# Performance work log

Hardware: AMD Instinct MI355X
Metric: run time of the kernel (lower is better)

## Reference

```python
import jax, jax.numpy as jnp
import numpy as np

N_NODES = 100000
N_EDGES = 800000
IN_DIM = 128
HID = 128
N_CLASSES = 4


def setup_inputs() -> dict:
    key = jax.random.key(0)
    ks = jax.random.split(key, 8)
    x = jax.random.normal(ks[0], (N_NODES, IN_DIM), dtype=jnp.float32)
    edge_index = jax.random.randint(ks[1], (2, N_EDGES), 0, N_NODES, dtype=jnp.int32)
    s0 = 1.0 / np.sqrt(IN_DIM)
    s1 = 1.0 / np.sqrt(HID)
    W0 = jax.random.uniform(ks[2], (HID, IN_DIM), minval=-s0, maxval=s0, dtype=jnp.float32)
    b0 = jax.random.uniform(ks[3], (HID,), minval=-s0, maxval=s0, dtype=jnp.float32)
    W1 = jax.random.uniform(ks[4], (HID, HID), minval=-s1, maxval=s1, dtype=jnp.float32)
    b1 = jax.random.uniform(ks[5], (HID,), minval=-s1, maxval=s1, dtype=jnp.float32)
    Wc = jax.random.uniform(ks[6], (N_CLASSES, HID), minval=-s1, maxval=s1, dtype=jnp.float32)
    bc = jax.random.uniform(ks[7], (N_CLASSES,), minval=-s1, maxval=s1, dtype=jnp.float32)
    return {"x": x, "edge_index": edge_index, "W0": W0, "b0": b0,
            "W1": W1, "b1": b1, "Wc": Wc, "bc": bc}


def reference(x, edge_index, W0, b0, W1, b1, Wc, bc):
    row, col = edge_index[0], edge_index[1]
    n = x.shape[0]
    # layer 0: Linear + ReLU (dropout is identity in eval)
    h = jax.nn.relu(x @ W0.T + b0)                                  # [N, HID]
    # scatter-add neighbor aggregation with degree normalization
    agg = jax.ops.segment_sum(h[col], row, num_segments=n)          # [N, HID]
    deg = jax.ops.segment_sum(jnp.ones_like(row, dtype=h.dtype), row, num_segments=n)
    agg = agg / jnp.clip(deg, 1.0)[:, None]
    h = h + agg                                                     # residual add
    # final conv + ReLU + classifier
    h = jax.nn.relu(h @ W1.T + b1)
    logits = h @ Wc.T + bc                                          # [N, N_CLASSES]
    return logits
```

## Files before the change

kernel.cpp:

```cpp
#include <hip/hip_runtime.h>

#define IN_DIM 128
#define HID    128
#define NCLS   4

typedef __attribute__((ext_vector_type(8))) short bf16x8;
typedef __attribute__((ext_vector_type(4))) float f32x4;

__device__ inline ushort f2bf(float x) {
    uint u = __builtin_bit_cast(uint, x);
    u += 0x7FFFu + ((u >> 16) & 1u);
    return (ushort)(u >> 16);
}
__device__ inline float bf2f(ushort h) {
    uint u = ((uint)h) << 16;
    return __builtin_bit_cast(float, u);
}

__device__ inline void gload_lds16(const void* g, void* l) {
    __builtin_amdgcn_global_load_lds((const __attribute__((address_space(1))) void*)g,
                                     (__attribute__((address_space(3))) void*)l, 16, 0, 0);
}

__global__ __launch_bounds__(256) void cast_w(const float* __restrict__ W0,
                                              const float* __restrict__ W1,
                                              ushort* __restrict__ w0h, ushort* __restrict__ w0l,
                                              ushort* __restrict__ w1h, ushort* __restrict__ w1l)
{
    int i = blockIdx.x * 256 + threadIdx.x;
    float v = (i < 16384) ? W0[i] : W1[i - 16384];
    ushort h = f2bf(v);
    ushort l = f2bf(v - bf2f(h));
    if (i < 16384) { w0h[i] = h; w0l[i] = l; }
    else           { w1h[i - 16384] = h; w1l[i - 16384] = l; }
}


__device__ __forceinline__ void lin0_body(const float* __restrict__ X,
                                          const ushort* __restrict__ Whi,
                                          const ushort* __restrict__ Wlo,
                                          const float* __restrict__ Bv,
                                          ushort* __restrict__ Hhi,
                                          ushort* __restrict__ Hlo,
                                          int M, int bm, char* lds)
{
    const int tid = threadIdx.x;

    {
        const int row  = tid >> 2;
        const int seg  = tid & 3;
        const int grow = min(bm + row, M - 1);
        const float4* src = (const float4*)((const char*)X + (size_t)grow * 512 + seg * 128);
        float4 v[8];
        #pragma unroll
        for (int j = 0; j < 8; ++j) v[j] = src[j];

        #pragma unroll
        for (int j = 0; j < 4; ++j) {
            uint hw[4], lw[4];
            #pragma unroll
            for (int q = 0; q < 2; ++q) {
                const float4 f = v[j * 2 + q];
                ushort h0 = f2bf(f.x), h1 = f2bf(f.y), h2 = f2bf(f.z), h3 = f2bf(f.w);
                ushort l0 = f2bf(f.x - bf2f(h0)), l1 = f2bf(f.y - bf2f(h1));
                ushort l2 = f2bf(f.z - bf2f(h2)), l3 = f2bf(f.w - bf2f(h3));
                hw[q * 2]     = (uint)h0 | ((uint)h1 << 16);
                hw[q * 2 + 1] = (uint)h2 | ((uint)h3 << 16);
                lw[q * 2]     = (uint)l0 | ((uint)l1 << 16);
                lw[q * 2 + 1] = (uint)l2 | ((uint)l3 << 16);
            }
            int unit = (seg * 4 + j) ^ (row & 7);
            int off  = row * 256 + unit * 16;
            *(uint4*)(lds + off)         = make_uint4(hw[0], hw[1], hw[2], hw[3]);
            *(uint4*)(lds + 16384 + off) = make_uint4(lw[0], lw[1], lw[2], lw[3]);
        }
    }
    __syncthreads();

    const int wid = tid >> 6, lane = tid & 63;
    const int wr = wid >> 1, wc = wid & 1;
    const int colbase = wc * 64;
    const int lr = lane & 15, lk = lane >> 4;

    f32x4 acc[4][2];
    #pragma unroll
    for (int nt = 0; nt < 4; ++nt)
        #pragma unroll
        for (int rt = 0; rt < 2; ++rt) acc[nt][rt] = (f32x4){0.f, 0.f, 0.f, 0.f};

    #pragma unroll
    for (int kt = 0; kt < 4; ++kt) {
        const int ko = kt * 32 + lk * 8;
        bf16x8 xh[2], xl[2];
        #pragma unroll
        for (int rt = 0; rt < 2; ++rt) {
            int lrow = wr * 32 + rt * 16 + lr;
            int unit = (kt * 4 + lk) ^ (lrow & 7);
            int off  = lrow * 256 + unit * 16;
            xh[rt] = *(const bf16x8*)(lds + off);
            xl[rt] = *(const bf16x8*)(lds + 16384 + off);
        }
        #pragma unroll
        for (int nt = 0; nt < 4; ++nt) {
            size_t bo = (size_t)(colbase + nt * 16 + lr) * 128 + ko;
            bf16x8 wh = *(const bf16x8*)(Whi + bo);
            bf16x8 wl = *(const bf16x8*)(Wlo + bo);
            #pragma unroll
            for (int rt = 0; rt < 2; ++rt) {
                acc[nt][rt] = __builtin_amdgcn_mfma_f32_16x16x32_bf16(wh, xh[rt], acc[nt][rt], 0, 0, 0);
                acc[nt][rt] = __builtin_amdgcn_mfma_f32_16x16x32_bf16(wh, xl[rt], acc[nt][rt], 0, 0, 0);
                acc[nt][rt] = __builtin_amdgcn_mfma_f32_16x16x32_bf16(wl, xh[rt], acc[nt][rt], 0, 0, 0);
            }
        }
    }

    #pragma unroll
    for (int nt = 0; nt < 4; ++nt) {
        const int col0 = colbase + nt * 16 + lk * 4;
        const float4 bv4 = *(const float4*)(Bv + col0);
        const float bvv[4] = {bv4.x, bv4.y, bv4.z, bv4.w};
        #pragma unroll
        for (int rt = 0; rt < 2; ++rt) {
            int row = bm + wr * 32 + rt * 16 + lr;
            float o0 = fmaxf(acc[nt][rt][0] + bvv[0], 0.f);
            float o1 = fmaxf(acc[nt][rt][1] + bvv[1], 0.f);
            float o2 = fmaxf(acc[nt][rt][2] + bvv[2], 0.f);
            float o3 = fmaxf(acc[nt][rt][3] + bvv[3], 0.f);
            ushort4 h4, l4;
            h4.x = f2bf(o0); l4.x = f2bf(o0 - bf2f(h4.x));
            h4.y = f2bf(o1); l4.y = f2bf(o1 - bf2f(h4.y));
            h4.z = f2bf(o2); l4.z = f2bf(o2 - bf2f(h4.z));
            h4.w = f2bf(o3); l4.w = f2bf(o3 - bf2f(h4.w));
            size_t oo = (size_t)row * 128 + col0;
            *(ushort4*)(Hhi + oo) = h4;
            *(ushort4*)(Hlo + oo) = l4;
        }
    }
}

__global__ __launch_bounds__(256) void k_lin0_count(const float* __restrict__ X,
                                                    const ushort* __restrict__ Whi,
                                                    const ushort* __restrict__ Wlo,
                                                    const float* __restrict__ Bv,
                                                    ushort* __restrict__ Hhi,
                                                    ushort* __restrict__ Hlo, int M,
                                                    int nLin0,
                                                    const int* __restrict__ rows,
                                                    int* __restrict__ deg, int E)
{
    __shared__ uint4 lds4[2048];
    if ((int)blockIdx.x < nLin0) {
        lin0_body(X, Whi, Wlo, Bv, Hhi, Hlo, M, blockIdx.x * 64, (char*)lds4);
    } else {
        int e = (blockIdx.x - nLin0) * 256 + threadIdx.x;
        if (e < E) atomicAdd(&deg[rows[e]], 1);
    }
}

__global__ __launch_bounds__(256) void k_lin0_fill(const float* __restrict__ X,
                                                   const ushort* __restrict__ Whi,
                                                   const ushort* __restrict__ Wlo,
                                                   const float* __restrict__ Bv,
                                                   ushort* __restrict__ Hhi,
                                                   ushort* __restrict__ Hlo, int M,
                                                   int nLin0, int baseLin0,
                                                   const int* __restrict__ rows,
                                                   const int* __restrict__ cols,
                                                   int* __restrict__ pos,
                                                   int* __restrict__ col_sorted, int E)
{
    __shared__ uint4 lds4[2048];
    if ((int)blockIdx.x < nLin0) {
        lin0_body(X, Whi, Wlo, Bv, Hhi, Hlo, M, (baseLin0 + blockIdx.x) * 64, (char*)lds4);
    } else {
        int e = (blockIdx.x - nLin0) * 256 + threadIdx.x;
        if (e < E) {
            int p = atomicAdd(&pos[rows[e]], 1);
            __builtin_nontemporal_store(cols[e], &col_sorted[p]);
        }
    }
}

__global__ __launch_bounds__(256) void gnn_lin1_mfma(const ushort* __restrict__ Ahi,
                                                     const ushort* __restrict__ Alo,
                                                     const ushort* __restrict__ Whi,
                                                     const ushort* __restrict__ Wlo,
                                                     const float* __restrict__ Bv,
                                                     const float* __restrict__ Wc,
                                                     const float* __restrict__ bc,
                                                     float* __restrict__ Out, int M)
{
    __shared__ uint4 lds4[2048];
    __shared__ float red[2][64][4];
    char* lds = (char*)lds4;

    const int tid = threadIdx.x;
    const int wid = tid >> 6, lane = tid & 63;
    const int bm  = blockIdx.x * 64;

    #pragma unroll
    for (int i = 0; i < 8; ++i) {
        int o = wid * 8192 + i * 1024 + lane * 16;
        const ushort* plane = (o < 16384) ? Ahi : Alo;
        int po   = o & 16383;
        int row  = po >> 8;
        int unit = (po >> 4) & 15;
        const char* src = (const char*)plane + (size_t)(bm + row) * 256
                        + ((unit ^ (row & 7)) << 4);
        gload_lds16(src, lds + wid * 8192 + i * 1024);
    }
    __syncthreads();

    const int wr = wid >> 1, wc = wid & 1;
    const int colbase = wc * 64;
    const int lr = lane & 15, lk = lane >> 4;

    f32x4 acc[4][2];
    #pragma unroll
    for (int nt = 0; nt < 4; ++nt)
        #pragma unroll
        for (int rt = 0; rt < 2; ++rt) acc[nt][rt] = (f32x4){0.f, 0.f, 0.f, 0.f};

    #pragma unroll
    for (int kt = 0; kt < 4; ++kt) {
        const int ko = kt * 32 + lk * 8;
        bf16x8 xh[2], xl[2];
        #pragma unroll
        for (int rt = 0; rt < 2; ++rt) {
            int lrow = wr * 32 + rt * 16 + lr;
            int unit = (kt * 4 + lk) ^ (lrow & 7);
            int off  = lrow * 256 + unit * 16;
            xh[rt] = *(const bf16x8*)(lds + off);
            xl[rt] = *(const bf16x8*)(lds + 16384 + off);
        }
        #pragma unroll
        for (int nt = 0; nt < 4; ++nt) {
            size_t bo = (size_t)(colbase + nt * 16 + lr) * 128 + ko;
            bf16x8 wh = *(const bf16x8*)(Whi + bo);
            bf16x8 wl = *(const bf16x8*)(Wlo + bo);
            #pragma unroll
            for (int rt = 0; rt < 2; ++rt) {
                acc[nt][rt] = __builtin_amdgcn_mfma_f32_16x16x32_bf16(wh, xh[rt], acc[nt][rt], 0, 0, 0);
                acc[nt][rt] = __builtin_amdgcn_mfma_f32_16x16x32_bf16(wh, xl[rt], acc[nt][rt], 0, 0, 0);
                acc[nt][rt] = __builtin_amdgcn_mfma_f32_16x16x32_bf16(wl, xh[rt], acc[nt][rt], 0, 0, 0);
            }
        }
    }

    float p[2][4] = {{0.f, 0.f, 0.f, 0.f}, {0.f, 0.f, 0.f, 0.f}};
    #pragma unroll
    for (int nt = 0; nt < 4; ++nt) {
        const int col0 = colbase + nt * 16 + lk * 4;
        const float4 bv4 = *(const float4*)(Bv + col0);
        const float bvv[4] = {bv4.x, bv4.y, bv4.z, bv4.w};
        float4 wcr[4];
        #pragma unroll
        for (int c = 0; c < 4; ++c) wcr[c] = *(const float4*)(Wc + c * HID + col0);
        #pragma unroll
        for (int rt = 0; rt < 2; ++rt) {
            float h2v[4];
            #pragma unroll
            for (int r = 0; r < 4; ++r) h2v[r] = fmaxf(acc[nt][rt][r] + bvv[r], 0.f);
            #pragma unroll
            for (int c = 0; c < 4; ++c) {
                const float* w = (const float*)&wcr[c];
                p[rt][c] = fmaf(h2v[0], w[0], p[rt][c]);
                p[rt][c] = fmaf(h2v[1], w[1], p[rt][c]);
                p[rt][c] = fmaf(h2v[2], w[2], p[rt][c]);
                p[rt][c] = fmaf(h2v[3], w[3], p[rt][c]);
            }
        }
    }
    #pragma unroll
    for (int offs = 16; offs < 64; offs <<= 1)
        #pragma unroll
        for (int rt = 0; rt < 2; ++rt)
            #pragma unroll
            for (int c = 0; c < 4; ++c)
                p[rt][c] += __shfl_xor(p[rt][c], offs);

    if (lk == 0) {
        #pragma unroll
        for (int rt = 0; rt < 2; ++rt) {
            f32x4 v = {p[rt][0], p[rt][1], p[rt][2], p[rt][3]};
            *(f32x4*)&red[wc][wr * 32 + rt * 16 + lr][0] = v;
        }
    }
    __syncthreads();

    const int row_local = tid >> 2, cls = tid & 3;
    int row = blockIdx.x * 64 + row_local;
    if (row < M) {
        float s = bc[cls] + red[0][row_local][cls] + red[1][row_local][cls];
        Out[(size_t)row * 4 + cls] = s;
    }
}

__global__ __launch_bounds__(256) void scan_blocks(const int* __restrict__ deg,
                                                   int* __restrict__ off,
                                                   int* __restrict__ bsum, int M)
{
    __shared__ int sh[256];
    int i = blockIdx.x * 256 + threadIdx.x;
    int v = (i < M) ? deg[i] : 0;
    sh[threadIdx.x] = v;
    __syncthreads();
    #pragma unroll
    for (int d = 1; d < 256; d <<= 1) {
        int t = (threadIdx.x >= d) ? sh[threadIdx.x - d] : 0;
        __syncthreads();
        sh[threadIdx.x] += t;
        __syncthreads();
    }
    if (i < M) off[i] = sh[threadIdx.x] - v;
    if (threadIdx.x == 255) bsum[blockIdx.x] = sh[255];
}

__global__ __launch_bounds__(512) void scan_bsum(int* __restrict__ bsum, int NB)
{
    __shared__ int sh[512];
    int v = (threadIdx.x < NB) ? bsum[threadIdx.x] : 0;
    sh[threadIdx.x] = v;
    __syncthreads();
    #pragma unroll
    for (int d = 1; d < 512; d <<= 1) {
        int t = (threadIdx.x >= d) ? sh[threadIdx.x - d] : 0;
        __syncthreads();
        sh[threadIdx.x] += t;
        __syncthreads();
    }
    if (threadIdx.x < NB) bsum[threadIdx.x] = sh[threadIdx.x] - v;
}

__global__ __launch_bounds__(256) void add_off(int* __restrict__ off,
                                               const int* __restrict__ bsum,
                                               int* __restrict__ pos, int M)
{
    int i = blockIdx.x * 256 + threadIdx.x;
    if (i < M) {
        int o = off[i] + bsum[i >> 8];
        off[i] = o;
        pos[i] = o;
    }
}

__global__ __launch_bounds__(256) void gnn_aggregate(const ushort* __restrict__ Hhi,
                                                     const ushort* __restrict__ Hlo,
                                                     const int* __restrict__ off,
                                                     const int* __restrict__ deg,
                                                     const int* __restrict__ col_sorted,
                                                     ushort* __restrict__ InHi,
                                                     ushort* __restrict__ InLo,
                                                     int M, int Mpad)
{
    int gid  = blockIdx.x * 8 + (threadIdx.x >> 5);
    int lane = threadIdx.x & 31;
    if (gid >= Mpad) return;
    size_t oidx = (size_t)gid * 32 + lane;
    if (gid >= M) {
        ((ushort4*)InHi)[oidx] = make_ushort4(0, 0, 0, 0);
        ((ushort4*)InLo)[oidx] = make_ushort4(0, 0, 0, 0);
        return;
    }

    const ushort4* G = (const ushort4*)Hhi;
    int start = off[gid];
    int d     = deg[gid];
    int end   = start + d;

    float s0[4] = {0.f, 0.f, 0.f, 0.f};
    float s1[4] = {0.f, 0.f, 0.f, 0.f};
    float s2[4] = {0.f, 0.f, 0.f, 0.f};
    float s3[4] = {0.f, 0.f, 0.f, 0.f};
    int e = start;
    for (; e + 4 <= end; e += 4) {
        int c0 = col_sorted[e], c1 = col_sorted[e + 1];
        int c2 = col_sorted[e + 2], c3 = col_sorted[e + 3];
        ushort4 g0 = G[(size_t)c0 * 32 + lane];
        ushort4 g1 = G[(size_t)c1 * 32 + lane];
        ushort4 g2 = G[(size_t)c2 * 32 + lane];
        ushort4 g3 = G[(size_t)c3 * 32 + lane];
        s0[0] += bf2f(g0.x); s0[1] += bf2f(g0.y); s0[2] += bf2f(g0.z); s0[3] += bf2f(g0.w);
        s1[0] += bf2f(g1.x); s1[1] += bf2f(g1.y); s1[2] += bf2f(g1.z); s1[3] += bf2f(g1.w);
        s2[0] += bf2f(g2.x); s2[1] += bf2f(g2.y); s2[2] += bf2f(g2.z); s2[3] += bf2f(g2.w);
        s3[0] += bf2f(g3.x); s3[1] += bf2f(g3.y); s3[2] += bf2f(g3.z); s3[3] += bf2f(g3.w);
    }
    for (; e < end; ++e) {
        int c0 = col_sorted[e];
        ushort4 g0 = G[(size_t)c0 * 32 + lane];
        s0[0] += bf2f(g0.x); s0[1] += bf2f(g0.y); s0[2] += bf2f(g0.z); s0[3] += bf2f(g0.w);
    }
    float a0 = (s0[0] + s1[0]) + (s2[0] + s3[0]);
    float a1 = (s0[1] + s1[1]) + (s2[1] + s3[1]);
    float a2 = (s0[2] + s1[2]) + (s2[2] + s3[2]);
    float a3 = (s0[3] + s1[3]) + (s2[3] + s3[3]);

    float inv = 1.0f / fmaxf((float)d, 1.0f);
    ushort4 rh = ((const ushort4*)Hhi)[oidx];
    ushort4 rl = ((const ushort4*)Hlo)[oidx];
    float o0 = bf2f(rh.x) + bf2f(rl.x) + a0 * inv;
    float o1 = bf2f(rh.y) + bf2f(rl.y) + a1 * inv;
    float o2 = bf2f(rh.z) + bf2f(rl.z) + a2 * inv;
    float o3 = bf2f(rh.w) + bf2f(rl.w) + a3 * inv;

    ushort4 h4, l4;
    h4.x = f2bf(o0); l4.x = f2bf(o0 - bf2f(h4.x));
    h4.y = f2bf(o1); l4.y = f2bf(o1 - bf2f(h4.y));
    h4.z = f2bf(o2); l4.z = f2bf(o2 - bf2f(h4.z));
    h4.w = f2bf(o3); l4.w = f2bf(o3 - bf2f(h4.w));
    ((ushort4*)InHi)[oidx] = h4;
    ((ushort4*)InLo)[oidx] = l4;
}

extern "C" void kernel_launch(void* const* d_in, const int* in_sizes, int n_in,
                              void* d_out, int out_size, void* d_ws, size_t ws_size,
                              hipStream_t stream)
{
    const float* x  = (const float*)d_in[0];
    const int*   ei = (const int*)  d_in[1];
    const float* W0 = (const float*)d_in[2];
    const float* b0 = (const float*)d_in[3];
    const float* W1 = (const float*)d_in[4];
    const float* b1 = (const float*)d_in[5];
    const float* Wc = (const float*)d_in[6];
    const float* bc = (const float*)d_in[7];
    float* out = (float*)d_out;

    const int M    = in_sizes[0] / IN_DIM;
    const int E    = in_sizes[1] / 2;
    const int Mpad = (M + 63) & ~63;
    const int NB   = (M + 255) / 256;

    ushort* Hhi  = (ushort*)d_ws;
    ushort* Hlo  = Hhi  + (size_t)Mpad * 128;
    ushort* InHi = Hlo  + (size_t)Mpad * 128;
    ushort* InLo = InHi + (size_t)Mpad * 128;
    ushort* W0h  = InLo + (size_t)Mpad * 128;
    ushort* W0l  = W0h + 16384;
    ushort* W1h  = W0l + 16384;
    ushort* W1l  = W1h + 16384;
    int* deg_i   = (int*)(W1l + 16384);
    int* off     = deg_i + M;
    int* pos     = off + M;
    int* bsum    = pos + M;
    int* col_sorted = bsum + 512;

    const int* rows = ei;
    const int* cols = ei + E;

    hipMemsetAsync(deg_i, 0, (size_t)M * sizeof(int), stream);

    const int gridMM = Mpad / 64;
    const int nA     = (gridMM + 1) / 2;
    const int nB     = gridMM - nA;
    const int gridE  = (E + 255) / 256;
    const int gridN  = (M + 255) / 256;

    cast_w<<<128, 256, 0, stream>>>(W0, W1, W0h, W0l, W1h, W1l);

    k_lin0_count<<<nA + gridE, 256, 0, stream>>>(x, W0h, W0l, b0, Hhi, Hlo, M,
                                                 nA, rows, deg_i, E);

    scan_blocks<<<gridN, 256, 0, stream>>>(deg_i, off, bsum, M);
    scan_bsum<<<1, 512, 0, stream>>>(bsum, NB);
    add_off<<<gridN, 256, 0, stream>>>(off, bsum, pos, M);

    k_lin0_fill<<<nB + gridE, 256, 0, stream>>>(x, W0h, W0l, b0, Hhi, Hlo, M,
                                                nB, nA, rows, cols, pos, col_sorted, E);

    gnn_aggregate<<<(Mpad + 7) / 8, 256, 0, stream>>>(Hhi, Hlo, off, deg_i, col_sorted,
                                                      InHi, InLo, M, Mpad);
    gnn_lin1_mfma<<<gridMM, 256, 0, stream>>>(InHi, InLo, W1h, W1l, b1, Wc, bc, out, M);
}
```

Measured before the change: 295.9 us.

## Replace three-kernel prefix scan with single atomic-cursor wave-level offset allocation

Replaces the three-pass exclusive scan (block scan, block-sum scan, add offsets) with one kernel. Each wave scans its 64 degrees with shuffles and reserves a contiguous range from a global atomic cursor, so CSR segments are no longer in node order but stay contiguous per node. This removes two kernel launches and their serial dependency. It also hardcodes the lin0 split to 1250 blocks and drops the nontemporal store on col_sorted.

```diff
diff --git a/kernel.cpp b/kernel.cpp
--- a/kernel.cpp
+++ b/kernel.cpp
@@ -157,6 +157,30 @@
     }
 }
 
+__global__ __launch_bounds__(256) void alloc_off(const int* __restrict__ deg,
+                                                 int* __restrict__ off,
+                                                 int* __restrict__ pos,
+                                                 int* __restrict__ cursor, int M)
+{
+    int i = blockIdx.x * 256 + threadIdx.x;
+    int lane = threadIdx.x & 63;
+    int d = (i < M) ? deg[i] : 0;
+    int v = d;
+    #pragma unroll
+    for (int o = 1; o < 64; o <<= 1) {
+        int t = __shfl_up(v, o);
+        if (lane >= o) v += t;
+    }
+    int b = 0;
+    if (lane == 63) b = atomicAdd(cursor, v);
+    b = __shfl(b, 63);
+    if (i < M) {
+        int o = b + v - d;
+        off[i] = o;
+        pos[i] = o;
+    }
+}
+
 __global__ __launch_bounds__(256) void k_lin0_fill(const float* __restrict__ X,
                                                    const ushort* __restrict__ Whi,
                                                    const ushort* __restrict__ Wlo,
@@ -176,7 +200,7 @@
         int e = (blockIdx.x - nLin0) * 256 + threadIdx.x;
         if (e < E) {
             int p = atomicAdd(&pos[rows[e]], 1);
-            __builtin_nontemporal_store(cols[e], &col_sorted[p]);
+            col_sorted[p] = cols[e];
         }
     }
 }
@@ -293,54 +317,6 @@
     if (row < M) {
         float s = bc[cls] + red[0][row_local][cls] + red[1][row_local][cls];
         Out[(size_t)row * 4 + cls] = s;
-    }
-}
-
-__global__ __launch_bounds__(256) void scan_blocks(const int* __restrict__ deg,
-                                                   int* __restrict__ off,
-                                                   int* __restrict__ bsum, int M)
-{
-    __shared__ int sh[256];
-    int i = blockIdx.x * 256 + threadIdx.x;
-    int v = (i < M) ? deg[i] : 0;
-    sh[threadIdx.x] = v;
-    __syncthreads();
-    #pragma unroll
-    for (int d = 1; d < 256; d <<= 1) {
-        int t = (threadIdx.x >= d) ? sh[threadIdx.x - d] : 0;
-        __syncthreads();
-        sh[threadIdx.x] += t;
-        __syncthreads();
-    }
-    if (i < M) off[i] = sh[threadIdx.x] - v;
-    if (threadIdx.x == 255) bsum[blockIdx.x] = sh[255];
-}
-
-__global__ __launch_bounds__(512) void scan_bsum(int* __restrict__ bsum, int NB)
-{
-    __shared__ int sh[512];
-    int v = (threadIdx.x < NB) ? bsum[threadIdx.x] : 0;
-    sh[threadIdx.x] = v;
-    __syncthreads();
-    #pragma unroll
-    for (int d = 1; d < 512; d <<= 1) {
-        int t = (threadIdx.x >= d) ? sh[threadIdx.x - d] : 0;
-        __syncthreads();
-        sh[threadIdx.x] += t;
-        __syncthreads();
-    }
-    if (threadIdx.x < NB) bsum[threadIdx.x] = sh[threadIdx.x] - v;
-}
-
-__global__ __launch_bounds__(256) void add_off(int* __restrict__ off,
-                                               const int* __restrict__ bsum,
-                                               int* __restrict__ pos, int M)
-{
-    int i = blockIdx.x * 256 + threadIdx.x;
-    if (i < M) {
-        int o = off[i] + bsum[i >> 8];
-        off[i] = o;
-        pos[i] = o;
     }
 }
 
@@ -429,7 +405,6 @@
     const int M    = in_sizes[0] / IN_DIM;
     const int E    = in_sizes[1] / 2;
     const int Mpad = (M + 63) & ~63;
-    const int NB   = (M + 255) / 256;
 
     ushort* Hhi  = (ushort*)d_ws;
     ushort* Hlo  = Hhi  + (size_t)Mpad * 128;
@@ -440,18 +415,18 @@
     ushort* W1h  = W0l + 16384;
     ushort* W1l  = W1h + 16384;
     int* deg_i   = (int*)(W1l + 16384);
-    int* off     = deg_i + M;
+    int* cursor  = deg_i + M;
+    int* off     = cursor + 16;
     int* pos     = off + M;
-    int* bsum    = pos + M;
-    int* col_sorted = bsum + 512;
+    int* col_sorted = pos + M;
 
     const int* rows = ei;
     const int* cols = ei + E;
 
-    hipMemsetAsync(deg_i, 0, (size_t)M * sizeof(int), stream);
+    hipMemsetAsync(deg_i, 0, (size_t)(M + 16) * sizeof(int), stream);
 
     const int gridMM = Mpad / 64;
-    const int nA     = (gridMM + 1) / 2;
+    const int nA     = 1250;
     const int nB     = gridMM - nA;
     const int gridE  = (E + 255) / 256;
     const int gridN  = (M + 255) / 256;
@@ -461,9 +436,7 @@
     k_lin0_count<<<nA + gridE, 256, 0, stream>>>(x, W0h, W0l, b0, Hhi, Hlo, M,
                                                  nA, rows, deg_i, E);
 
-    scan_blocks<<<gridN, 256, 0, stream>>>(deg_i, off, bsum, M);
-    scan_bsum<<<1, 512, 0, stream>>>(bsum, NB);
-    add_off<<<gridN, 256, 0, stream>>>(off, bsum, pos, M);
+    alloc_off<<<gridN, 256, 0, stream>>>(deg_i, off, pos, cursor, M);
 
     k_lin0_fill<<<nB + gridE, 256, 0, stream>>>(x, W0h, W0l, b0, Hhi, Hlo, M,
                                                 nB, nA, rows, cols, pos, col_sorted, E);
```

Measured after the change: 312.2 us. +5.5%, slower.
